# Optimization experiments

Measured on AMD Instinct MI355X. Metric: run time of the kernel, lower is better.

## Reference

```python
import jax, jax.numpy as jnp
import numpy as np

C = 256
EPS = 1e-5


def setup_inputs() -> dict:
    key = jax.random.key(0)
    ks = jax.random.split(key, 10)
    B, H, W = 4, 64, 64
    x1 = jax.random.normal(ks[0], (B, C, H, W), dtype=jnp.float32)
    x2 = jax.random.normal(ks[1], (B, C, H, W), dtype=jnp.float32)
    s = 1.0 / np.sqrt(C)
    qw = jax.random.normal(ks[2], (C, C), dtype=jnp.float32) * s
    qb = jax.random.normal(ks[3], (C,), dtype=jnp.float32) * 0.01
    kw = jax.random.normal(ks[4], (C, C), dtype=jnp.float32) * s
    kb = jax.random.normal(ks[5], (C,), dtype=jnp.float32) * 0.01
    vw = jax.random.normal(ks[6], (C, C), dtype=jnp.float32) * s
    vb = jax.random.normal(ks[7], (C,), dtype=jnp.float32) * 0.01
    ln_w = jnp.ones((C,), dtype=jnp.float32)
    ln_b = jnp.zeros((C,), dtype=jnp.float32)
    return {"x1": x1, "x2": x2, "qw": qw, "qb": qb, "kw": kw, "kb": kb,
            "vw": vw, "vb": vb, "ln_w": ln_w, "ln_b": ln_b}


def _conv1x1(x, w, b):
    # 1x1 conv == per-pixel matmul over channels. x: [B,C,H,W], w: [O,C]
    return jnp.einsum('oc,bchw->bohw', w, x) + b[None, :, None, None]


def reference(x1, x2, qw, qb, kw, kb, vw, vb, ln_w, ln_b):
    q = _conv1x1(x1, qw, qb)   # [B,C,H,W]
    k = _conv1x1(x2, kw, kb)   # [B,C,H,W]
    v = _conv1x1(x2, vw, vb)   # [B,C,H,W]
    # scores: [B,H,W,I,J]; softmax over LAST axis (j) only, as in the torch code
    scores = jnp.einsum('bchw,bcij->bhwij', q, k)
    attn = jax.nn.softmax(scores, axis=-1)
    fusion = jnp.einsum('bhwij,bcij->bchw', attn, v)  # [B,C,H,W]
    # LayerNorm2d: normalize over channel dim per spatial location
    mean = jnp.mean(fusion, axis=1, keepdims=True)
    var = jnp.var(fusion, axis=1, keepdims=True)
    normed = (fusion - mean) * jax.lax.rsqrt(var + EPS)
    return normed * ln_w[None, :, None, None] + ln_b[None, :, None, None]
```

## Files before the change

kernel.cpp:

```cpp
#include <hip/hip_runtime.h>


#define CDIM 256
#define NPOS 4096
#define BATCH 4
#define EPSV 1e-5f

typedef _Float16 f16;
typedef __attribute__((ext_vector_type(4))) _Float16 f16x4;
typedef __attribute__((ext_vector_type(8))) _Float16 f16x8;
typedef __attribute__((ext_vector_type(4))) float f32x4;
typedef __attribute__((ext_vector_type(16))) float f32x16;

#define WST       264
#define QK_STRIDE 264
#define V_STRIDE  72
#define DQ_STRIDE 72
#define F_STRIDE  68

#define LBAR() asm volatile("s_waitcnt lgkmcnt(0)\n\ts_barrier" ::: "memory")


static __device__ __forceinline__ f16x8 cvt8(const float* __restrict__ p) {
    float4 w0 = *(const float4*)p;
    float4 w1 = *(const float4*)(p + 4);
    f16x8 r;
    r[0] = (f16)w0.x; r[1] = (f16)w0.y; r[2] = (f16)w0.z; r[3] = (f16)w0.w;
    r[4] = (f16)w1.x; r[5] = (f16)w1.y; r[6] = (f16)w1.z; r[7] = (f16)w1.w;
    return r;
}

__global__ __launch_bounds__(256, 4) void wconv_kernel(
    const float* __restrict__ qw, const float* __restrict__ kw,
    const float* __restrict__ vw, f16* __restrict__ Wf)
{
    const int id = blockIdx.x;
    const int t  = threadIdx.x;
    const int pr = id >> 3;
    const int q  = (id >> 1) & 3;
    const int ot = id & 1;
    const float* W = (pr == 0 ? qw : pr == 1 ? kw : vw);
    f16* D = Wf + (size_t)id * 8192;
    #pragma unroll
    for (int i = 0; i < 4; ++i) {
        int idx = t + i * 256;
        int ks = idx >> 6, l = idx & 63;
        const float* src = W + (size_t)(q * 64 + ot * 32 + (l & 31)) * CDIM
                             + ks * 16 + (l >> 5) * 8;
        *(f16x8*)(D + (size_t)idx * 8) = cvt8(src);
    }
}

__global__ __launch_bounds__(256, 3) void gemm_kernel(
    const float* __restrict__ x1, const float* __restrict__ x2,
    const f16* __restrict__ Wf,
    const float* __restrict__ qb, const float* __restrict__ kb,
    const float* __restrict__ vb,
    f16* __restrict__ Qg, f16* __restrict__ Kg, f16* __restrict__ Vg)
{
    __shared__ f16 Xs[64 * WST];
    __shared__ f16 Ds[64 * DQ_STRIDE];
    __shared__ float biasS[256];

    const int id = blockIdx.x;
    const int pr  = id >> 8;
    const int rem = id & 255;
    const int b   = rem >> 6;
    const int p0  = (rem & 63) << 6;
    const float* xsrc = ((pr == 0) ? x1 : x2) + (size_t)b * CDIM * NPOS + p0;
    const float* bias = (pr == 0) ? qb : (pr == 1) ? kb : vb;

    const int t = threadIdx.x, w = t >> 6, l = t & 63, lm = l & 31, lh = l >> 5;
    const int pt = w & 1, ot = w >> 1;

    const f16* Wfp = Wf + (size_t)pr * 65536 + (size_t)ot * 8192;

    biasS[t] = bias[t];
    #pragma unroll
    for (int g = 0; g < 8; ++g) {
        f16x8 h;
        #pragma unroll
        for (int j = 0; j < 8; ++j)
            h[j] = (f16)xsrc[(size_t)(w * 64 + g * 8 + j) * NPOS + l];
        *(f16x8*)&Xs[l * WST + w * 64 + g * 8] = h;
    }

    f16x8 wf[16];
    #pragma unroll
    for (int ks = 0; ks < 16; ++ks)
        wf[ks] = *(const f16x8*)(Wfp + (size_t)ks * 512 + l * 8);

    __syncthreads();

    for (int q = 0; q < 4; ++q) {
        f32x16 accA = {}, accB = {};
        #pragma unroll
        for (int ks = 0; ks < 16; ks += 2) {
            f16x8 x0  = *(const f16x8*)&Xs[(pt * 32 + lm) * WST + ks * 16 + lh * 8];
            f16x8 x1v = *(const f16x8*)&Xs[(pt * 32 + lm) * WST + (ks + 1) * 16 + lh * 8];
            if (pr < 2) {
                accA = __builtin_amdgcn_mfma_f32_32x32x16_f16(x0, wf[ks], accA, 0, 0, 0);
                accB = __builtin_amdgcn_mfma_f32_32x32x16_f16(x1v, wf[ks + 1], accB, 0, 0, 0);
            } else {
                accA = __builtin_amdgcn_mfma_f32_32x32x16_f16(wf[ks], x0, accA, 0, 0, 0);
                accB = __builtin_amdgcn_mfma_f32_32x32x16_f16(wf[ks + 1], x1v, accB, 0, 0, 0);
            }
        }

        if (q < 3) {
            #pragma unroll
            for (int ks = 0; ks < 16; ++ks)
                wf[ks] = *(const f16x8*)(Wfp + (size_t)(q + 1) * 16384
                                             + (size_t)ks * 512 + l * 8);
        }

        if (pr < 2) {
            int o_l = ot * 32 + lm;
            float bv = biasS[q * 64 + o_l];
            #pragma unroll
            for (int r = 0; r < 16; ++r) {
                int p_l = pt * 32 + (r & 3) + 8 * (r >> 2) + 4 * lh;
                Ds[p_l * DQ_STRIDE + o_l] = (f16)(accA[r] + accB[r] + bv);
            }
        } else {
            #pragma unroll
            for (int r = 0; r < 16; ++r) {
                int o_l = ot * 32 + (r & 3) + 8 * (r >> 2) + 4 * lh;
                Ds[o_l * DQ_STRIDE + pt * 32 + lm] =
                    (f16)(accA[r] + accB[r] + biasS[q * 64 + o_l]);
            }
        }
        LBAR();

        #pragma unroll
        for (int j = 0; j < 2; ++j) {
            int row = (t >> 3) + j * 32;
            int cc  = (t & 7) * 8;
            f16x8 vdat = *(const f16x8*)&Ds[row * DQ_STRIDE + cc];
            if (pr < 2) {
                f16* Out = (pr == 0) ? Qg : Kg;
                *(f16x8*)(Out + ((size_t)(b * NPOS + p0 + row)) * CDIM + q * 64 + cc) = vdat;
            } else {
                *(f16x8*)(Vg + ((size_t)(b * CDIM + q * 64 + row)) * NPOS + p0 + cc) = vdat;
            }
        }
        LBAR();
    }
}

__global__ __launch_bounds__(256, 2) void attn_kernel(
    const f16* __restrict__ Qg, const f16* __restrict__ Kg, const f16* __restrict__ Vg,
    float* __restrict__ Fp)
{
    __shared__ f16   Ks[64 * QK_STRIDE];
    __shared__ f16   Vs[256 * V_STRIDE];
    __shared__ f16   Pl[64 * V_STRIDE];
    __shared__ float RedM[2][64], RedS[2][64];

    const int t    = threadIdx.x;
    const int L    = (int)((blockIdx.x & 7) * 64 + (blockIdx.x >> 3));
    const int grp  = L >> 6;
    const int b    = grp >> 1;
    const int half = grp & 1;
    const int qt   = L & 63;
    const int p0   = qt << 6;
    const int bq   = b * 64 + qt;
    const int w    = t >> 6;
    const int l    = t & 63;
    const int lm   = l & 31;
    const int lh   = l >> 5;
    const int spt  = w & 1;
    const int skt  = w >> 1;

    f16x8 qf[16];
    {
        const f16* qptr = Qg + (size_t)(b * NPOS + p0 + spt * 32 + lm) * CDIM + lh * 8;
        #pragma unroll
        for (int ks = 0; ks < 16; ++ks) qf[ks] = *(const f16x8*)(qptr + ks * 16);
    }

    const int kr = t >> 5, koff = (t & 31) * 8;
    f16x8 kreg[8];
    auto issue_k = [&](int ch) {
        const int i0 = ch * 64;
        #pragma unroll
        for (int r = 0; r < 8; ++r)
            kreg[r] = *(const f16x8*)(Kg + (size_t)(b * NPOS + i0 + r * 8 + kr) * CDIM + koff);
    };

    const int vr = t >> 3;
    const int vc = (t & 7) * 8;
    f16x8 vreg[8];
    auto issue_v = [&](int ch) {
        const int i0 = ch * 64;
        #pragma unroll
        for (int i = 0; i < 8; ++i)
            vreg[i] = *(const f16x8*)(Vg + (size_t)(b * CDIM + i * 32 + vr) * NPOS + i0 + vc);
    };

    issue_k(half * 32);
    issue_v(half * 32);

    f32x16 facc[4] = {};

    for (int it = 0; it < 32; ++it) {
        const int ch = half * 32 + it;

        #pragma unroll
        for (int r = 0; r < 8; ++r)
            *(f16x8*)&Ks[(r * 8 + kr) * QK_STRIDE + koff] = kreg[r];
        if (it < 31) issue_k(ch + 1);
        LBAR();

        #pragma unroll
        for (int i = 0; i < 8; ++i)
            *(f16x8*)&Vs[(i * 32 + vr) * V_STRIDE + vc] = vreg[i];
        if (it < 31) issue_v(ch + 1);

        f32x16 st = {};
        __builtin_amdgcn_s_setprio(1);
        #pragma unroll
        for (int ks = 0; ks < 16; ++ks) {
            f16x8 kf = *(const f16x8*)&Ks[(skt * 32 + lm) * QK_STRIDE + ks * 16 + lh * 8];
            st = __builtin_amdgcn_mfma_f32_32x32x16_f16(kf, qf[ks], st, 0, 0, 0);
        }
        __builtin_amdgcn_s_setprio(0);

        float mx = st[0];
        #pragma unroll
        for (int r = 1; r < 16; ++r) mx = fmaxf(mx, st[r]);
        mx = fmaxf(mx, __shfl_xor(mx, 32));
        float ss = 0.f;
        #pragma unroll
        for (int r = 0; r < 16; ++r) {
            float e = __expf(st[r] - mx);
            st[r] = e;
            ss += e;
        }
        ss += __shfl_xor(ss, 32);
        if (lh == 0) { RedM[skt][spt * 32 + lm] = mx; RedS[skt][spt * 32 + lm] = ss; }
        LBAR();

        float mo = RedM[skt ^ 1][spt * 32 + lm];
        float so = RedS[skt ^ 1][spt * 32 + lm];
        float M  = fmaxf(mx, mo);
        float S  = ss * __expf(mx - M) + so * __expf(mo - M);
        float scale = __expf(mx - M) * __builtin_amdgcn_rcpf(S);

        #pragma unroll
        for (int rq = 0; rq < 4; ++rq) {
            f16x4 pk;
            #pragma unroll
            for (int q2 = 0; q2 < 4; ++q2) pk[q2] = (f16)(st[rq * 4 + q2] * scale);
            *(f16x4*)&Pl[(spt * 32 + lm) * V_STRIDE + skt * 32 + rq * 8 + lh * 4] = pk;
        }
        LBAR();

        __builtin_amdgcn_s_setprio(1);
        #pragma unroll
        for (int kb = 0; kb < 4; ++kb) {
            f16x8 pf0 = *(const f16x8*)&Pl[lm * V_STRIDE + kb * 16 + lh * 8];
            f16x8 pf1 = *(const f16x8*)&Pl[(32 + lm) * V_STRIDE + kb * 16 + lh * 8];
            f16x8 va0 = *(const f16x8*)&Vs[(w * 64 + lm) * V_STRIDE + kb * 16 + lh * 8];
            f16x8 va1 = *(const f16x8*)&Vs[(w * 64 + 32 + lm) * V_STRIDE + kb * 16 + lh * 8];
            facc[0] = __builtin_amdgcn_mfma_f32_32x32x16_f16(va0, pf0, facc[0], 0, 0, 0);
            facc[1] = __builtin_amdgcn_mfma_f32_32x32x16_f16(va0, pf1, facc[1], 0, 0, 0);
            facc[2] = __builtin_amdgcn_mfma_f32_32x32x16_f16(va1, pf0, facc[2], 0, 0, 0);
            facc[3] = __builtin_amdgcn_mfma_f32_32x32x16_f16(va1, pf1, facc[3], 0, 0, 0);
        }
        __builtin_amdgcn_s_setprio(0);
    }

    float* dst = Fp + ((size_t)bq * 2 + half) * (CDIM * 64);
    #pragma unroll
    for (int ii = 0; ii < 2; ++ii)
        #pragma unroll
        for (int jj = 0; jj < 2; ++jj)
            #pragma unroll
            for (int r = 0; r < 16; ++r) {
                int c = w * 64 + ii * 32 + (r & 3) + 8 * (r >> 2) + 4 * lh;
                int p = jj * 32 + lm;
                dst[c * 64 + p] = facc[ii * 2 + jj][r];
            }
}

__global__ __launch_bounds__(256, 2) void merge_ln_kernel(
    const float* __restrict__ Fp, const float* __restrict__ ln_w,
    const float* __restrict__ ln_b, float* __restrict__ out)
{
    __shared__ float Fs[256 * F_STRIDE];
    __shared__ float redS[16 * 64], redQ[16 * 64];
    __shared__ float lnw_s[256], lnb_s[256];
    __shared__ float mu_s[64], rs_s[64];

    const int t  = threadIdx.x;
    const int bq = blockIdx.x;
    const int b  = bq >> 6;
    const int p0 = (bq & 63) << 6;

    lnw_s[t] = ln_w[t]; lnb_s[t] = ln_b[t];

    const int pb = (t & 15) * 4;
    const int cg = t >> 4;
    const float* base = Fp + (size_t)bq * 2 * (CDIM * 64);

    f32x4 s4 = {}, q4 = {};
    #pragma unroll 4
    for (int ci = 0; ci < 16; ++ci) {
        int c = cg * 16 + ci;
        size_t off = (size_t)c * 64 + pb;
        f32x4 v = *(const f32x4*)(base + off);
        v += *(const f32x4*)(base + (size_t)(CDIM * 64) + off);
        *(f32x4*)&Fs[c * F_STRIDE + pb] = v;
        s4 += v; q4 += v * v;
    }
    #pragma unroll
    for (int k2 = 0; k2 < 4; ++k2) {
        redS[cg * 64 + pb + k2] = s4[k2];
        redQ[cg * 64 + pb + k2] = q4[k2];
    }
    __syncthreads();
    if (t < 64) {
        float ss = 0.f, qq = 0.f;
        #pragma unroll
        for (int g2 = 0; g2 < 16; ++g2) { ss += redS[g2 * 64 + t]; qq += redQ[g2 * 64 + t]; }
        float mean = ss * (1.0f / 256.0f);
        float var  = qq * (1.0f / 256.0f) - mean * mean;
        mu_s[t] = mean;
        rs_s[t] = rsqrtf(var + EPSV);
    }
    __syncthreads();
    const int p   = t & 63;
    const int cg2 = t >> 6;
    const float mu = mu_s[p], rs = rs_s[p];
    float* dst = out + (size_t)b * CDIM * NPOS + p0 + p;
    #pragma unroll 4
    for (int ci = 0; ci < 64; ++ci) {
        int c = cg2 * 64 + ci;
        dst[(size_t)c * NPOS] = (Fs[c * F_STRIDE + p] - mu) * rs * lnw_s[c] + lnb_s[c];
    }
}

extern "C" void kernel_launch(void* const* d_in, const int* in_sizes, int n_in,
                              void* d_out, int out_size, void* d_ws, size_t ws_size,
                              hipStream_t stream)
{
    const float* x1  = (const float*)d_in[0];
    const float* x2  = (const float*)d_in[1];
    const float* qw  = (const float*)d_in[2];
    const float* qb  = (const float*)d_in[3];
    const float* kw  = (const float*)d_in[4];
    const float* kb  = (const float*)d_in[5];
    const float* vw  = (const float*)d_in[6];
    const float* vb  = (const float*)d_in[7];
    const float* lnw = (const float*)d_in[8];
    const float* lnb = (const float*)d_in[9];

    const size_t tsz = (size_t)BATCH * NPOS * CDIM;
    f16* Qg  = (f16*)d_ws;
    f16* Kg  = Qg + tsz;
    f16* Vg  = Kg + tsz;
    f16* Wf  = Vg + tsz;
    float* Fp = (float*)(Wf + 3 * CDIM * CDIM);

    wconv_kernel<<<24, 256, 0, stream>>>(qw, kw, vw, Wf);
    gemm_kernel<<<768, 256, 0, stream>>>(x1, x2, Wf, qb, kb, vb, Qg, Kg, Vg);
    attn_kernel<<<512, 256, 0, stream>>>(Qg, Kg, Vg, Fp);
    merge_ln_kernel<<<256, 256, 0, stream>>>(Fp, lnw, lnb, (float*)d_out);
}
```

Measured before the change: 210.9 us.

## Fuse K and V projections per block to share the x2 tile

The projection GEMM now launches one block per (batch, position tile) for Q and one for K+V together. The K+V block loads x2 once into shared memory and computes both projections, instead of two separate blocks each reloading and converting x2. This cuts global reads and fp32-to-fp16 conversion work. In exchange, K/V blocks do twice the work of Q blocks, hold twice the weight registers, and occupancy drops to two blocks per CU.

```diff
diff --git a/kernel.cpp b/kernel.cpp
--- a/kernel.cpp
+++ b/kernel.cpp
@@ -51,7 +51,7 @@
     }
 }
 
-__global__ __launch_bounds__(256, 3) void gemm_kernel(
+__global__ __launch_bounds__(256, 2) void gemm_kernel(
     const float* __restrict__ x1, const float* __restrict__ x2,
     const f16* __restrict__ Wf,
     const float* __restrict__ qb, const float* __restrict__ kb,
@@ -59,23 +59,40 @@
     f16* __restrict__ Qg, f16* __restrict__ Kg, f16* __restrict__ Vg)
 {
     __shared__ f16 Xs[64 * WST];
-    __shared__ f16 Ds[64 * DQ_STRIDE];
-    __shared__ float biasS[256];
-
-    const int id = blockIdx.x;
-    const int pr  = id >> 8;
-    const int rem = id & 255;
-    const int b   = rem >> 6;
-    const int p0  = (rem & 63) << 6;
-    const float* xsrc = ((pr == 0) ? x1 : x2) + (size_t)b * CDIM * NPOS + p0;
-    const float* bias = (pr == 0) ? qb : (pr == 1) ? kb : vb;
+    __shared__ f16 DsA[64 * DQ_STRIDE];
+    __shared__ f16 DsB[64 * DQ_STRIDE];
+    __shared__ float biasA[256], biasB[256];
+
+    const int id   = blockIdx.x;
+    const int isKV = id & 1;
+    const int rem  = id >> 1;
+    const int b    = rem >> 6;
+    const int p0   = (rem & 63) << 6;
+    const float* xsrc = (isKV ? x2 : x1) + (size_t)b * CDIM * NPOS + p0;
 
     const int t = threadIdx.x, w = t >> 6, l = t & 63, lm = l & 31, lh = l >> 5;
     const int pt = w & 1, ot = w >> 1;
 
-    const f16* Wfp = Wf + (size_t)pr * 65536 + (size_t)ot * 8192;
-
-    biasS[t] = bias[t];
+    if (isKV) { biasA[t] = kb[t]; biasB[t] = vb[t]; }
+    else      { biasA[t] = qb[t]; }
+
+    const f16* WfQ = Wf + (size_t)ot * 8192;
+    const f16* WfK = Wf + 65536  + (size_t)ot * 8192;
+    const f16* WfV = Wf + 131072 + (size_t)ot * 8192;
+
+    f16x8 wk[16], wv[16];
+    if (isKV) {
+        #pragma unroll
+        for (int ks = 0; ks < 16; ++ks) {
+            wk[ks] = *(const f16x8*)(WfK + (size_t)ks * 512 + l * 8);
+            wv[ks] = *(const f16x8*)(WfV + (size_t)ks * 512 + l * 8);
+        }
+    } else {
+        #pragma unroll
+        for (int ks = 0; ks < 16; ++ks)
+            wk[ks] = *(const f16x8*)(WfQ + (size_t)ks * 512 + l * 8);
+    }
+
     #pragma unroll
     for (int g = 0; g < 8; ++g) {
         f16x8 h;
@@ -84,67 +101,95 @@
             h[j] = (f16)xsrc[(size_t)(w * 64 + g * 8 + j) * NPOS + l];
         *(f16x8*)&Xs[l * WST + w * 64 + g * 8] = h;
     }
-
-    f16x8 wf[16];
-    #pragma unroll
-    for (int ks = 0; ks < 16; ++ks)
-        wf[ks] = *(const f16x8*)(Wfp + (size_t)ks * 512 + l * 8);
-
-    __syncthreads();
+    LBAR();
 
     for (int q = 0; q < 4; ++q) {
-        f32x16 accA = {}, accB = {};
-        #pragma unroll
-        for (int ks = 0; ks < 16; ks += 2) {
-            f16x8 x0  = *(const f16x8*)&Xs[(pt * 32 + lm) * WST + ks * 16 + lh * 8];
-            f16x8 x1v = *(const f16x8*)&Xs[(pt * 32 + lm) * WST + (ks + 1) * 16 + lh * 8];
-            if (pr < 2) {
-                accA = __builtin_amdgcn_mfma_f32_32x32x16_f16(x0, wf[ks], accA, 0, 0, 0);
-                accB = __builtin_amdgcn_mfma_f32_32x32x16_f16(x1v, wf[ks + 1], accB, 0, 0, 0);
-            } else {
-                accA = __builtin_amdgcn_mfma_f32_32x32x16_f16(wf[ks], x0, accA, 0, 0, 0);
-                accB = __builtin_amdgcn_mfma_f32_32x32x16_f16(wf[ks + 1], x1v, accB, 0, 0, 0);
-            }
-        }
-
-        if (q < 3) {
-            #pragma unroll
-            for (int ks = 0; ks < 16; ++ks)
-                wf[ks] = *(const f16x8*)(Wfp + (size_t)(q + 1) * 16384
-                                             + (size_t)ks * 512 + l * 8);
-        }
-
-        if (pr < 2) {
-            int o_l = ot * 32 + lm;
-            float bv = biasS[q * 64 + o_l];
-            #pragma unroll
-            for (int r = 0; r < 16; ++r) {
-                int p_l = pt * 32 + (r & 3) + 8 * (r >> 2) + 4 * lh;
-                Ds[p_l * DQ_STRIDE + o_l] = (f16)(accA[r] + accB[r] + bv);
-            }
+        if (!isKV) {
+            f32x16 accA = {}, accB = {};
+            #pragma unroll
+            for (int ks = 0; ks < 16; ks += 2) {
+                f16x8 x0  = *(const f16x8*)&Xs[(pt * 32 + lm) * WST + ks * 16 + lh * 8];
+                f16x8 x1v = *(const f16x8*)&Xs[(pt * 32 + lm) * WST + (ks + 1) * 16 + lh * 8];
+                accA = __builtin_amdgcn_mfma_f32_32x32x16_f16(x0, wk[ks], accA, 0, 0, 0);
+                accB = __builtin_amdgcn_mfma_f32_32x32x16_f16(x1v, wk[ks + 1], accB, 0, 0, 0);
+            }
+            if (q < 3) {
+                #pragma unroll
+                for (int ks = 0; ks < 16; ++ks)
+                    wk[ks] = *(const f16x8*)(WfQ + (size_t)(q + 1) * 16384
+                                                 + (size_t)ks * 512 + l * 8);
+            }
+            {
+                int o_l = ot * 32 + lm;
+                float bv = biasA[q * 64 + o_l];
+                #pragma unroll
+                for (int r = 0; r < 16; ++r) {
+                    int p_l = pt * 32 + (r & 3) + 8 * (r >> 2) + 4 * lh;
+                    DsA[p_l * DQ_STRIDE + o_l] = (f16)(accA[r] + accB[r] + bv);
+                }
+            }
+            LBAR();
+            #pragma unroll
+            for (int j = 0; j < 2; ++j) {
+                int row = (t >> 3) + j * 32;
+                int cc  = (t & 7) * 8;
+                f16x8 vd = *(const f16x8*)&DsA[row * DQ_STRIDE + cc];
+                *(f16x8*)(Qg + ((size_t)(b * NPOS + p0 + row)) * CDIM + q * 64 + cc) = vd;
+            }
+            LBAR();
         } else {
+            f32x16 accA = {}, accB = {};
+            #pragma unroll
+            for (int ks = 0; ks < 16; ks += 2) {
+                f16x8 x0  = *(const f16x8*)&Xs[(pt * 32 + lm) * WST + ks * 16 + lh * 8];
+                f16x8 x1v = *(const f16x8*)&Xs[(pt * 32 + lm) * WST + (ks + 1) * 16 + lh * 8];
+                accA = __builtin_amdgcn_mfma_f32_32x32x16_f16(x0, wk[ks], accA, 0, 0, 0);
+                accB = __builtin_amdgcn_mfma_f32_32x32x16_f16(x1v, wk[ks + 1], accB, 0, 0, 0);
+            }
+            {
+                int o_l = ot * 32 + lm;
+                float bv = biasA[q * 64 + o_l];
+                #pragma unroll
+                for (int r = 0; r < 16; ++r) {
+                    int p_l = pt * 32 + (r & 3) + 8 * (r >> 2) + 4 * lh;
+                    DsA[p_l * DQ_STRIDE + o_l] = (f16)(accA[r] + accB[r] + bv);
+                }
+            }
+            f32x16 accC = {}, accD = {};
+            #pragma unroll
+            for (int ks = 0; ks < 16; ks += 2) {
+                f16x8 x0  = *(const f16x8*)&Xs[(pt * 32 + lm) * WST + ks * 16 + lh * 8];
+                f16x8 x1v = *(const f16x8*)&Xs[(pt * 32 + lm) * WST + (ks + 1) * 16 + lh * 8];
+                accC = __builtin_amdgcn_mfma_f32_32x32x16_f16(wv[ks], x0, accC, 0, 0, 0);
+                accD = __builtin_amdgcn_mfma_f32_32x32x16_f16(wv[ks + 1], x1v, accD, 0, 0, 0);
+            }
+            if (q < 3) {
+                #pragma unroll
+                for (int ks = 0; ks < 16; ++ks) {
+                    wk[ks] = *(const f16x8*)(WfK + (size_t)(q + 1) * 16384
+                                                 + (size_t)ks * 512 + l * 8);
+                    wv[ks] = *(const f16x8*)(WfV + (size_t)(q + 1) * 16384
+                                                 + (size_t)ks * 512 + l * 8);
+                }
+            }
             #pragma unroll
             for (int r = 0; r < 16; ++r) {
                 int o_l = ot * 32 + (r & 3) + 8 * (r >> 2) + 4 * lh;
-                Ds[o_l * DQ_STRIDE + pt * 32 + lm] =
-                    (f16)(accA[r] + accB[r] + biasS[q * 64 + o_l]);
-            }
-        }
-        LBAR();
-
-        #pragma unroll
-        for (int j = 0; j < 2; ++j) {
-            int row = (t >> 3) + j * 32;
-            int cc  = (t & 7) * 8;
-            f16x8 vdat = *(const f16x8*)&Ds[row * DQ_STRIDE + cc];
-            if (pr < 2) {
-                f16* Out = (pr == 0) ? Qg : Kg;
-                *(f16x8*)(Out + ((size_t)(b * NPOS + p0 + row)) * CDIM + q * 64 + cc) = vdat;
-            } else {
-                *(f16x8*)(Vg + ((size_t)(b * CDIM + q * 64 + row)) * NPOS + p0 + cc) = vdat;
-            }
-        }
-        LBAR();
+                DsB[o_l * DQ_STRIDE + pt * 32 + lm] =
+                    (f16)(accC[r] + accD[r] + biasB[q * 64 + o_l]);
+            }
+            LBAR();
+            #pragma unroll
+            for (int j = 0; j < 2; ++j) {
+                int row = (t >> 3) + j * 32;
+                int cc  = (t & 7) * 8;
+                f16x8 vk = *(const f16x8*)&DsA[row * DQ_STRIDE + cc];
+                f16x8 vv = *(const f16x8*)&DsB[row * DQ_STRIDE + cc];
+                *(f16x8*)(Kg + ((size_t)(b * NPOS + p0 + row)) * CDIM + q * 64 + cc) = vk;
+                *(f16x8*)(Vg + ((size_t)(b * CDIM + q * 64 + row)) * NPOS + p0 + cc) = vv;
+            }
+            LBAR();
+        }
     }
 }
 
@@ -258,11 +303,11 @@
 
         __builtin_amdgcn_s_setprio(1);
         #pragma unroll
-        for (int kb = 0; kb < 4; ++kb) {
-            f16x8 pf0 = *(const f16x8*)&Pl[lm * V_STRIDE + kb * 16 + lh * 8];
-            f16x8 pf1 = *(const f16x8*)&Pl[(32 + lm) * V_STRIDE + kb * 16 + lh * 8];
-            f16x8 va0 = *(const f16x8*)&Vs[(w * 64 + lm) * V_STRIDE + kb * 16 + lh * 8];
-            f16x8 va1 = *(const f16x8*)&Vs[(w * 64 + 32 + lm) * V_STRIDE + kb * 16 + lh * 8];
+        for (int kb2 = 0; kb2 < 4; ++kb2) {
+            f16x8 pf0 = *(const f16x8*)&Pl[lm * V_STRIDE + kb2 * 16 + lh * 8];
+            f16x8 pf1 = *(const f16x8*)&Pl[(32 + lm) * V_STRIDE + kb2 * 16 + lh * 8];
+            f16x8 va0 = *(const f16x8*)&Vs[(w * 64 + lm) * V_STRIDE + kb2 * 16 + lh * 8];
+            f16x8 va1 = *(const f16x8*)&Vs[(w * 64 + 32 + lm) * V_STRIDE + kb2 * 16 + lh * 8];
             facc[0] = __builtin_amdgcn_mfma_f32_32x32x16_f16(va0, pf0, facc[0], 0, 0, 0);
             facc[1] = __builtin_amdgcn_mfma_f32_32x32x16_f16(va0, pf1, facc[1], 0, 0, 0);
             facc[2] = __builtin_amdgcn_mfma_f32_32x32x16_f16(va1, pf0, facc[2], 0, 0, 0);
@@ -364,7 +409,7 @@
     float* Fp = (float*)(Wf + 3 * CDIM * CDIM);
 
     wconv_kernel<<<24, 256, 0, stream>>>(qw, kw, vw, Wf);
-    gemm_kernel<<<768, 256, 0, stream>>>(x1, x2, Wf, qb, kb, vb, Qg, Kg, Vg);
+    gemm_kernel<<<512, 256, 0, stream>>>(x1, x2, Wf, qb, kb, vb, Qg, Kg, Vg);
     attn_kernel<<<512, 256, 0, stream>>>(Qg, Kg, Vg, Fp);
     merge_ln_kernel<<<256, 256, 0, stream>>>(Fp, lnw, lnb, (float*)d_out);
 }
```

New measurement: 242.5 us. +15.0%, slower.

## Fuse split-K merge and LayerNorm into attention kernel via flag handoff

Applied to the files above, without the earlier changes.

Removes the separate merge_ln kernel. Within each pair of attention blocks that share a query tile, one half writes its partial result to global memory and sets a release flag. The other half spins on that flag, adds the partial into its registers, and computes LayerNorm plus the final store directly. This saves one kernel launch and halves the partial-buffer traffic. It depends on both halves of a pair being co-resident, since a consumer spinning while its producer is not yet scheduled could deadlock.

```diff
diff --git a/kernel.cpp b/kernel.cpp
--- a/kernel.cpp
+++ b/kernel.cpp
@@ -16,7 +16,6 @@
 #define QK_STRIDE 264
 #define V_STRIDE  72
 #define DQ_STRIDE 72
-#define F_STRIDE  68
 
 #define LBAR() asm volatile("s_waitcnt lgkmcnt(0)\n\ts_barrier" ::: "memory")
 
@@ -32,10 +31,11 @@
 
 __global__ __launch_bounds__(256, 4) void wconv_kernel(
     const float* __restrict__ qw, const float* __restrict__ kw,
-    const float* __restrict__ vw, f16* __restrict__ Wf)
+    const float* __restrict__ vw, f16* __restrict__ Wf, int* __restrict__ flags)
 {
     const int id = blockIdx.x;
     const int t  = threadIdx.x;
+    if (id == 0) flags[t] = 0;
     const int pr = id >> 3;
     const int q  = (id >> 1) & 3;
     const int ot = id & 1;
@@ -150,7 +150,8 @@
 
 __global__ __launch_bounds__(256, 2) void attn_kernel(
     const f16* __restrict__ Qg, const f16* __restrict__ Kg, const f16* __restrict__ Vg,
-    float* __restrict__ Fp)
+    const float* __restrict__ ln_w, const float* __restrict__ ln_b,
+    float* __restrict__ Fp, int* __restrict__ flags, float* __restrict__ out)
 {
     __shared__ f16   Ks[64 * QK_STRIDE];
     __shared__ f16   Vs[256 * V_STRIDE];
@@ -271,74 +272,101 @@
         __builtin_amdgcn_s_setprio(0);
     }
 
-    float* dst = Fp + ((size_t)bq * 2 + half) * (CDIM * 64);
+    int* flag = flags + bq;
+    const int isCons = (half == (qt & 1));
+
+    if (!isCons) {
+        float* dst = Fp + (size_t)bq * (CDIM * 64);
+        #pragma unroll
+        for (int ii = 0; ii < 2; ++ii)
+            #pragma unroll
+            for (int jj = 0; jj < 2; ++jj)
+                #pragma unroll
+                for (int r = 0; r < 16; ++r) {
+                    int c = w * 64 + ii * 32 + (r & 3) + 8 * (r >> 2) + 4 * lh;
+                    int p = jj * 32 + lm;
+                    dst[c * 64 + p] = facc[ii * 2 + jj][r];
+                }
+        __syncthreads();
+        if (t == 0) {
+            __threadfence();
+            __hip_atomic_store(flag, 1, __ATOMIC_RELEASE, __HIP_MEMORY_SCOPE_AGENT);
+        }
+        return;
+    }
+
+    if (t == 0) {
+        while (__hip_atomic_load(flag, __ATOMIC_ACQUIRE, __HIP_MEMORY_SCOPE_AGENT) == 0)
+            __builtin_amdgcn_s_sleep(2);
+    }
+    __syncthreads();
+
+    {
+        const float* src = Fp + (size_t)bq * (CDIM * 64);
+        #pragma unroll
+        for (int ii = 0; ii < 2; ++ii)
+            #pragma unroll
+            for (int jj = 0; jj < 2; ++jj)
+                #pragma unroll
+                for (int r = 0; r < 16; ++r) {
+                    int c = w * 64 + ii * 32 + (r & 3) + 8 * (r >> 2) + 4 * lh;
+                    int p = jj * 32 + lm;
+                    facc[ii * 2 + jj][r] += src[c * 64 + p];
+                }
+    }
+
+    float* scr   = (float*)&Ks[0];
+    float* lnS   = scr;
+    float* lnQ   = scr + 256;
+    float* mu_s  = scr + 512;
+    float* rs_s  = scr + 576;
+    float* lnw_s = scr + 640;
+    float* lnb_s = scr + 896;
+
+    lnw_s[t] = ln_w[t];
+    lnb_s[t] = ln_b[t];
+
+    float ps0 = 0.f, pq0 = 0.f, ps1 = 0.f, pq1 = 0.f;
     #pragma unroll
     for (int ii = 0; ii < 2; ++ii)
         #pragma unroll
-        for (int jj = 0; jj < 2; ++jj)
+        for (int r = 0; r < 16; ++r) {
+            float a  = facc[ii * 2 + 0][r];
+            float c2 = facc[ii * 2 + 1][r];
+            ps0 += a;  pq0 += a * a;
+            ps1 += c2; pq1 += c2 * c2;
+        }
+    ps0 += __shfl_xor(ps0, 32); pq0 += __shfl_xor(pq0, 32);
+    ps1 += __shfl_xor(ps1, 32); pq1 += __shfl_xor(pq1, 32);
+    if (lh == 0) {
+        lnS[w * 64 + lm] = ps0;       lnQ[w * 64 + lm] = pq0;
+        lnS[w * 64 + 32 + lm] = ps1;  lnQ[w * 64 + 32 + lm] = pq1;
+    }
+    __syncthreads();
+    if (t < 64) {
+        float ssum = lnS[t] + lnS[64 + t] + lnS[128 + t] + lnS[192 + t];
+        float qsum = lnQ[t] + lnQ[64 + t] + lnQ[128 + t] + lnQ[192 + t];
+        float mean = ssum * (1.0f / 256.0f);
+        float var  = qsum * (1.0f / 256.0f) - mean * mean;
+        mu_s[t] = mean;
+        rs_s[t] = rsqrtf(var + EPSV);
+    }
+    __syncthreads();
+
+    float* o0 = out + (size_t)b * CDIM * NPOS + p0;
+    #pragma unroll
+    for (int ii = 0; ii < 2; ++ii)
+        #pragma unroll
+        for (int jj = 0; jj < 2; ++jj) {
+            int p = jj * 32 + lm;
+            float mu = mu_s[p], rs = rs_s[p];
             #pragma unroll
             for (int r = 0; r < 16; ++r) {
                 int c = w * 64 + ii * 32 + (r & 3) + 8 * (r >> 2) + 4 * lh;
-                int p = jj * 32 + lm;
-                dst[c * 64 + p] = facc[ii * 2 + jj][r];
-            }
-}
-
-__global__ __launch_bounds__(256, 2) void merge_ln_kernel(
-    const float* __restrict__ Fp, const float* __restrict__ ln_w,
-    const float* __restrict__ ln_b, float* __restrict__ out)
-{
-    __shared__ float Fs[256 * F_STRIDE];
-    __shared__ float redS[16 * 64], redQ[16 * 64];
-    __shared__ float lnw_s[256], lnb_s[256];
-    __shared__ float mu_s[64], rs_s[64];
-
-    const int t  = threadIdx.x;
-    const int bq = blockIdx.x;
-    const int b  = bq >> 6;
-    const int p0 = (bq & 63) << 6;
-
-    lnw_s[t] = ln_w[t]; lnb_s[t] = ln_b[t];
-
-    const int pb = (t & 15) * 4;
-    const int cg = t >> 4;
-    const float* base = Fp + (size_t)bq * 2 * (CDIM * 64);
-
-    f32x4 s4 = {}, q4 = {};
-    #pragma unroll 4
-    for (int ci = 0; ci < 16; ++ci) {
-        int c = cg * 16 + ci;
-        size_t off = (size_t)c * 64 + pb;
-        f32x4 v = *(const f32x4*)(base + off);
-        v += *(const f32x4*)(base + (size_t)(CDIM * 64) + off);
-        *(f32x4*)&Fs[c * F_STRIDE + pb] = v;
-        s4 += v; q4 += v * v;
-    }
-    #pragma unroll
-    for (int k2 = 0; k2 < 4; ++k2) {
-        redS[cg * 64 + pb + k2] = s4[k2];
-        redQ[cg * 64 + pb + k2] = q4[k2];
-    }
-    __syncthreads();
-    if (t < 64) {
-        float ss = 0.f, qq = 0.f;
-        #pragma unroll
-        for (int g2 = 0; g2 < 16; ++g2) { ss += redS[g2 * 64 + t]; qq += redQ[g2 * 64 + t]; }
-        float mean = ss * (1.0f / 256.0f);
-        float var  = qq * (1.0f / 256.0f) - mean * mean;
-        mu_s[t] = mean;
-        rs_s[t] = rsqrtf(var + EPSV);
-    }
-    __syncthreads();
-    const int p   = t & 63;
-    const int cg2 = t >> 6;
-    const float mu = mu_s[p], rs = rs_s[p];
-    float* dst = out + (size_t)b * CDIM * NPOS + p0 + p;
-    #pragma unroll 4
-    for (int ci = 0; ci < 64; ++ci) {
-        int c = cg2 * 64 + ci;
-        dst[(size_t)c * NPOS] = (Fs[c * F_STRIDE + p] - mu) * rs * lnw_s[c] + lnb_s[c];
-    }
+                o0[(size_t)c * NPOS + p] =
+                    (facc[ii * 2 + jj][r] - mu) * rs * lnw_s[c] + lnb_s[c];
+            }
+        }
 }
 
 extern "C" void kernel_launch(void* const* d_in, const int* in_sizes, int n_in,
@@ -362,9 +390,10 @@
     f16* Vg  = Kg + tsz;
     f16* Wf  = Vg + tsz;
     float* Fp = (float*)(Wf + 3 * CDIM * CDIM);
-
-    wconv_kernel<<<24, 256, 0, stream>>>(qw, kw, vw, Wf);
+    int* flags = (int*)(Fp + (size_t)256 * CDIM * 64);
+
+    wconv_kernel<<<24, 256, 0, stream>>>(qw, kw, vw, Wf, flags);
     gemm_kernel<<<768, 256, 0, stream>>>(x1, x2, Wf, qb, kb, vb, Qg, Kg, Vg);
-    attn_kernel<<<512, 256, 0, stream>>>(Qg, Kg, Vg, Fp);
-    merge_ln_kernel<<<256, 256, 0, stream>>>(Fp, lnw, lnb, (float*)d_out);
-}
+    attn_kernel<<<512, 256, 0, stream>>>(Qg, Kg, Vg, lnw, lnb, Fp, flags,
+                                         (float*)d_out);
+}
```

Result: slower. 227.5 us (+7.8%).
